# Kernel tuning notes

Measured on AMD Instinct MI355X. Metric: run time of the kernel, lower is better.

The kernel has to match this reference:

```python
import jax, jax.numpy as jnp
import numpy as np

# ---- config (matches init_kwargs) ----
B, CIN, IMG = 4, 3, 129
PATCH, STRIDE, PAD = 4, 1, 1
DIM = CIN * PATCH * PATCH          # 48, Token_performer input dim
EMB = 256                          # out_channel -> in_dim -> emb
M = EMB // 2                       # kernel_ratio=0.5 random features
UP = 2                             # up_scale
EPS = 1e-8


def layernorm(x, g, b):
    mu = x.mean(-1, keepdims=True)
    var = ((x - mu) ** 2).mean(-1, keepdims=True)
    return (x - mu) / jnp.sqrt(var + 1e-5) * g + b


def unfold(x, k=PATCH, pad=PAD):
    # torch nn.Unfold, stride=1: output [B, C*k*k, L*L], channel order (c, kh, kw)
    Bs, C, H, W = x.shape
    xp = jnp.pad(x, ((0, 0), (0, 0), (pad, pad), (pad, pad)))
    L = H + 2 * pad - k + 1
    cols = jnp.stack([xp[:, :, i:i + L, j:j + L]
                      for i in range(k) for j in range(k)], axis=2)  # [B,C,k*k,L,L]
    return cols.reshape(Bs, C * k * k, L * L)


def prm_exp(x, w):
    # Performer positive random features: exp(w@x - |x|^2/2)/sqrt(m)
    xd = 0.5 * jnp.sum(x * x, axis=-1, keepdims=True)          # [B,T,1]
    wtx = jnp.einsum('btd,md->btm', x, w)                       # [B,T,M]
    return jnp.exp(wtx - xd) / jnp.sqrt(jnp.float32(w.shape[0]))


def upsample_bilinear_ac(x, scale):
    # nn.UpsamplingBilinear2d => align_corners=True
    Bs, C, H, W = x.shape
    Ho, Wo = H * scale, W * scale
    def coords(n_in, n_out):
        f = jnp.arange(n_out, dtype=jnp.float32) * (n_in - 1) / (n_out - 1)
        i0 = jnp.clip(jnp.floor(f).astype(jnp.int32), 0, n_in - 2)
        return i0, f - i0.astype(jnp.float32)
    h0, th = coords(H, Ho)
    w0, tw = coords(W, Wo)
    xh = x[:, :, h0, :] * (1 - th)[None, None, :, None] + x[:, :, h0 + 1, :] * th[None, None, :, None]
    return xh[:, :, :, w0] * (1 - tw) + xh[:, :, :, w0 + 1] * tw


def setup_inputs() -> dict:
    key = jax.random.key(0)
    ks = jax.random.split(key, 8)
    def n(k, shape, s=0.02):
        return jax.random.normal(k, shape, dtype=jnp.float32) * s
    return dict(
        x=jax.random.normal(ks[0], (B, CIN, IMG, IMG), dtype=jnp.float32),
        g1=jnp.ones((DIM,), jnp.float32), b1=jnp.zeros((DIM,), jnp.float32),
        w_kqv=n(ks[1], (DIM, 3 * EMB)), b_kqv=jnp.zeros((3 * EMB,), jnp.float32),
        w_prm=jax.random.normal(ks[2], (M, EMB), dtype=jnp.float32) * 0.7,  # ~ orthogonal*sqrt(m)
        w_proj=n(ks[3], (EMB, EMB)), b_proj=jnp.zeros((EMB,), jnp.float32),
        g2=jnp.ones((EMB,), jnp.float32), b2=jnp.zeros((EMB,), jnp.float32),
        w_mlp1=n(ks[4], (EMB, EMB)), b_mlp1=jnp.zeros((EMB,), jnp.float32),
        w_mlp2=n(ks[5], (EMB, EMB)), b_mlp2=jnp.zeros((EMB,), jnp.float32),
    )


def reference(x, g1, b1, w_kqv, b_kqv, w_prm, w_proj, b_proj, g2, b2,
              w_mlp1, b_mlp1, w_mlp2, b_mlp2):
    Bs = x.shape[0]
    t = unfold(x).transpose(0, 2, 1)                     # [B, T, DIM], T = 128*128
    h = layernorm(t, g1, b1)
    kqv = h @ w_kqv + b_kqv                              # [B, T, 3*EMB]
    k, q, v = jnp.split(kqv, 3, axis=-1)                 # torch split order: k, q, v
    kp, qp = prm_exp(k, w_prm), prm_exp(q, w_prm)        # [B, T, M]
    D = jnp.einsum('btm,bm->bt', qp, kp.sum(axis=1))[..., None]   # [B,T,1]
    kptv = jnp.einsum('btn,btm->bnm', v, kp)             # [B, EMB, M]
    y = jnp.einsum('btm,bnm->btn', qp, kptv) / (D + EPS) # [B, T, EMB]
    y = v + (y @ w_proj + b_proj)                        # skip uses v
    z = layernorm(y, g2, b2)
    y = y + (jax.nn.gelu(z @ w_mlp1 + b_mlp1, approximate=False) @ w_mlp2 + b_mlp2)
    T = y.shape[1]
    S = int(np.sqrt(T))
    img = y.transpose(0, 2, 1).reshape(Bs, EMB, S, S)    # [B, 256, 128, 128]
    return upsample_bilinear_ac(img, UP)                 # [B, 256, 256, 256]
```

## Files before the change

kernel.cpp:

```cpp
#include <hip/hip_runtime.h>
#include <math.h>

#define TOK   16384
#define DIM   48
#define EMB   256
#define MF    128
#define IMGsz 129

typedef __attribute__((ext_vector_type(8))) short    bf16x8;
typedef __attribute__((ext_vector_type(8))) unsigned short u16x8;
typedef __attribute__((ext_vector_type(4))) unsigned short u16x4;
typedef __attribute__((ext_vector_type(4))) float    f32x4;

__device__ __forceinline__ ushort f2bf(float f) {
    union { float f; unsigned u; } v; v.f = f;
    unsigned u = v.u;
    return (ushort)((u + 0x7fffu + ((u >> 16) & 1u)) >> 16);
}
__device__ __forceinline__ float bf2f(ushort h) {
    union { unsigned u; float f; } v; v.u = ((unsigned)h) << 16; return v.f;
}

#define SWZ64(r,c)  ((r)*64  + (((((c)>>3) ^ ((r)&7)) & 7) << 3) + ((c)&7))
#define SWZ256(r,c) ((r)*256 + (((((c)>>3) ^ ((r)&7))) << 3) + ((c)&7))

__device__ __forceinline__ int fragmajor(int n, int k, int KC) {
    return (((n >> 4)*KC + (k >> 5))*4 + ((k >> 3) & 3))*128 + (n & 15)*8 + (k & 7);
}

__global__ __launch_bounds__(256) void kprep(
    const float* __restrict__ w_kqv, const float* __restrict__ b_kqv,
    const float* __restrict__ w_prm,
    const float* __restrict__ w_mlp1, const float* __restrict__ w_mlp2,
    ushort* __restrict__ Wbig, ushort* __restrict__ wT2, float* __restrict__ bkq)
{
    __shared__ float redp[64][4];
    int blk = blockIdx.x, tid = threadIdx.x;
    if (blk < 256) {
        if (tid < 64) {
            float v = (tid < DIM) ? w_kqv[tid*768 + 512 + blk] : 0.f;
            Wbig[fragmajor(blk, tid, 2)] = f2bf(v);
        }
    } else if (blk < 512) {
        int isQ = (blk >= 384);
        int m = blk - (isQ ? 384 : 256);
        int d = tid & 63, part = tid >> 6;
        float s = 0.f;
        if (d < 48) {
            const float* wr = w_kqv + d*768 + (isQ ? 256 : 0);
            const float* pr = w_prm + m*256;
            for (int n = part*64; n < part*64 + 64; n++) s += wr[n]*pr[n];
        }
        redp[d][part] = s;
        __syncthreads();
        if (tid < 64)
            Wbig[fragmajor((isQ ? 384 : 256) + m, tid, 2)] =
                f2bf(redp[tid][0]+redp[tid][1]+redp[tid][2]+redp[tid][3]);
    } else if (blk < 640) {
        int isQ = (blk >= 576);
        int j = blk - (isQ ? 576 : 512);
        int i = tid & 63, part = tid >> 6;
        int off = isQ ? 256 : 0;
        float s = 0.f;
        for (int n = part*64; n < part*64 + 64; n++) {
            float wi = (i < 48) ? w_kqv[i*768 + off + n] : (i == 48 ? b_kqv[off + n] : 0.f);
            float wj = (j < 48) ? w_kqv[j*768 + off + n] : (j == 48 ? b_kqv[off + n] : 0.f);
            s += wi*wj;
        }
        redp[i][part] = s;
        __syncthreads();
        if (tid < 64)
            Wbig[fragmajor((isQ ? 576 : 512) + j, tid, 2)] =
                f2bf(redp[tid][0]+redp[tid][1]+redp[tid][2]+redp[tid][3]);
    } else if (blk < 1152) {
        int w = (blk >= 896);
        int n = blk - (w ? 896 : 640);
        const float* src = w ? w_mlp2 : w_mlp1;
        wT2[w*65536 + fragmajor(n, tid, 8)] = f2bf(src[tid*256 + n]);
    } else {
        float s = 0.f;
        int m = tid & 127, off = (tid >= 128) ? 256 : 0;
        for (int n = 0; n < 256; n++) s += w_prm[m*256 + n]*b_kqv[off + n];
        bkq[tid] = s;
    }
}

__global__ __launch_bounds__(256, 3) void k1_mfma(
    const float* __restrict__ x, const float* __restrict__ g1, const float* __restrict__ b1,
    const ushort* __restrict__ Wbig, const float* __restrict__ b_kqv,
    const float* __restrict__ bkq,
    ushort* __restrict__ vfrag_out, ushort* __restrict__ kpT_out, ushort* __restrict__ qp_out)
{
    __shared__ __align__(16) ushort h_bf[32*64];
    __shared__ __align__(16) ushort vt_bf[32*256];
    __shared__ float xdp[4][32][2];
    __shared__ float xd2[32][2];
    __shared__ float red1[32][8], red2[32][8];
    __shared__ float mu_s[32], iv_s[32];
    float* t_s = (float*)vt_bf;

    const int blk = blockIdx.x;
    const int b  = blk >> 9;
    const int t0 = (blk & 511) << 5;
    const int tid = threadIdx.x;
    const int wid = tid >> 6;
    const int l15 = tid & 15, l4 = (tid >> 4) & 3;

    for (int e = tid; e < 32*DIM; e += 256) {
        int tok = e / DIM, j = e - tok*DIM;
        int t = t0 + tok;
        int lh = t >> 7, lw = t & 127;
        int c = j >> 4, kh = (j >> 2) & 3, kw = j & 3;
        int ih = lh + kh - 1, iw = lw + kw - 1;
        float val = 0.f;
        if (ih >= 0 && ih < IMGsz && iw >= 0 && iw < IMGsz)
            val = x[((b*3 + c)*IMGsz + ih)*IMGsz + iw];
        t_s[tok*DIM + j] = val;
    }
    __syncthreads();

    {
        int tg = tid >> 3, sl = tid & 7;
        const float* tr = &t_s[tg*DIM + sl*6];
        float s1 = 0.f, s2 = 0.f;
        #pragma unroll
        for (int j = 0; j < 6; j++) { float a = tr[j]; s1 += a; s2 = fmaf(a, a, s2); }
        red1[tg][sl] = s1; red2[tg][sl] = s2;
        __syncthreads();
        if (tid < 32) {
            float a = 0.f, q = 0.f;
            #pragma unroll
            for (int j = 0; j < 8; j++) { a += red1[tid][j]; q += red2[tid][j]; }
            float mu = a * (1.f/DIM);
            mu_s[tid] = mu;
            iv_s[tid] = rsqrtf(q*(1.f/DIM) - mu*mu + 1e-5f);
        }
        __syncthreads();
        float mu = mu_s[tg], iv = iv_s[tg];
        float hv[6];
        #pragma unroll
        for (int j = 0; j < 6; j++) hv[j] = (tr[j]-mu)*iv;
        #pragma unroll
        for (int j = 0; j < 6; j++) {
            int c = sl*6 + j;
            h_bf[SWZ64(tg, c)] = f2bf(hv[j]*g1[c] + b1[c]);
        }
        int c0 = 48 + sl*2;
        h_bf[SWZ64(tg, c0    )] = (sl == 0) ? (ushort)0x3F80 : (ushort)0;
        h_bf[SWZ64(tg, c0 + 1)] = 0;
    }
    __syncthreads();

    f32x4 acc[10][2];
    #pragma unroll
    for (int j = 0; j < 10; j++)
        #pragma unroll
        for (int m = 0; m < 2; m++) { acc[j][m][0]=0.f; acc[j][m][1]=0.f; acc[j][m][2]=0.f; acc[j][m][3]=0.f; }
    #pragma unroll
    for (int kc = 0; kc < 2; kc++) {
        int ch = ((kc*4 + l4) ^ (l15 & 7)) << 3;
        bf16x8 a0 = *(const bf16x8*)&h_bf[ l15      *64 + ch];
        bf16x8 a1 = *(const bf16x8*)&h_bf[(16 + l15)*64 + ch];
        #pragma unroll
        for (int j = 0; j < 10; j++) {
            int tile = wid + 4*j;
            bf16x8 bb = *(const bf16x8*)&Wbig[(((tile*2 + kc)*4 + l4)*16 + l15)*8];
            acc[j][0] = __builtin_amdgcn_mfma_f32_16x16x32_bf16(a0, bb, acc[j][0], 0, 0, 0);
            acc[j][1] = __builtin_amdgcn_mfma_f32_16x16x32_bf16(a1, bb, acc[j][1], 0, 0, 0);
        }
    }

    #pragma unroll
    for (int j = 0; j < 4; j++) {
        int col = (wid + 4*j)*16 + l15;
        float bias = b_kqv[512 + col];
        #pragma unroll
        for (int m = 0; m < 2; m++)
            #pragma unroll
            for (int r = 0; r < 4; r++) {
                int row = m*16 + l4*4 + r;
                vt_bf[row*256 + col] = f2bf(acc[j][m][r] + bias);
            }
    }
    #pragma unroll
    for (int m = 0; m < 2; m++)
        #pragma unroll
        for (int r = 0; r < 4; r++) {
            int row = m*16 + l4*4 + r;
            float hv = bf2f(h_bf[SWZ64(row, wid*16 + l15)]);
            float sk = acc[8][m][r]*hv, sq = acc[9][m][r]*hv;
            #pragma unroll
            for (int msk = 8; msk >= 1; msk >>= 1) {
                sk += __shfl_xor(sk, msk);
                sq += __shfl_xor(sq, msk);
            }
            if (l15 == 0) { xdp[wid][row][0] = sk; xdp[wid][row][1] = sq; }
        }
    __syncthreads();
    if (tid < 64) {
        int row = tid >> 1, ty = tid & 1;
        xd2[row][ty] = 0.5f*(xdp[0][row][ty] + xdp[1][row][ty] + xdp[2][row][ty] + xdp[3][row][ty]);
    }

    {
        ushort* dst = vfrag_out + (size_t)blk*8192 + tid*32;
        #pragma unroll
        for (int t8 = 0; t8 < 4; t8++) {
            u16x8 pk8;
            #pragma unroll
            for (int j = 0; j < 8; j++) pk8[j] = vt_bf[(t8*8 + j)*256 + tid];
            *(u16x8*)&dst[t8*8] = pk8;
        }
    }
    __syncthreads();

    const float scale = 0.08838834764831845f;
    #pragma unroll
    for (int j = 4; j < 6; j++) {
        int mcol = (wid + 4*j)*16 + l15 - 256;
        float bias = bkq[mcol];
        #pragma unroll
        for (int m = 0; m < 2; m++)
            #pragma unroll
            for (int r = 0; r < 4; r++) {
                int row = m*16 + l4*4 + r;
                vt_bf[row*256 + mcol] = f2bf(expf(acc[j][m][r] + bias - xd2[row][0]) * scale);
            }
    }
    #pragma unroll
    for (int j = 6; j < 8; j++) {
        int mcol = (wid + 4*j)*16 + l15 - 384;
        float bias = bkq[128 + mcol];
        #pragma unroll
        for (int m = 0; m < 2; m++)
            #pragma unroll
            for (int r = 0; r < 4; r++) {
                int row = m*16 + l4*4 + r;
                qp_out[(size_t)(b*TOK + t0 + row)*MF + mcol] =
                    f2bf(expf(acc[j][m][r] + bias - xd2[row][1]) * scale);
            }
    }
    __syncthreads();

    if (tid < 128) {
        ushort* dst = kpT_out + ((size_t)(b*MF + tid))*TOK + t0;
        #pragma unroll
        for (int t8 = 0; t8 < 4; t8++) {
            u16x8 pk8;
            #pragma unroll
            for (int j = 0; j < 8; j++) pk8[j] = vt_bf[(t8*8 + j)*256 + tid];
            *(u16x8*)&dst[t8*8] = pk8;
        }
    }
}

__global__ __launch_bounds__(256) void k2_ksum(const ushort* __restrict__ kpT, float* __restrict__ ksum)
{
    __shared__ float red[4];
    int blk = blockIdx.x;
    int b = blk >> 7, m = blk & 127;
    int tid = threadIdx.x;
    const ushort* row = kpT + (size_t)(b*MF + m)*TOK;
    float s = 0.f;
    for (int i = tid; i < TOK/8; i += 256) {
        u16x8 v = *(const u16x8*)&row[i*8];
        #pragma unroll
        for (int j = 0; j < 8; j++) s += bf2f(v[j]);
    }
    #pragma unroll
    for (int msk = 32; msk >= 1; msk >>= 1) s += __shfl_xor(s, msk);
    if ((tid & 63) == 0) red[tid >> 6] = s;
    __syncthreads();
    if (tid == 0) ksum[b*MF + m] = red[0] + red[1] + red[2] + red[3];
}

__global__ __launch_bounds__(256) void k3_kptv_mfma(
    const ushort* __restrict__ vfrag, const ushort* __restrict__ kpT, float* __restrict__ part)
{
    int blk = blockIdx.x;
    int b = blk >> 6, ns = (blk >> 5) & 1, kc = blk & 31;
    const int tid = threadIdx.x;
    const int wid = tid >> 6;
    const int l15 = tid & 15, l4 = (tid >> 4) & 3;
    const int t0 = kc * 512;
    const int n0 = ns*128 + wid*32;

    f32x4 acc[2][8];
    #pragma unroll
    for (int m = 0; m < 2; m++)
        #pragma unroll
        for (int n = 0; n < 8; n++) { acc[m][n][0]=0.f; acc[m][n][1]=0.f; acc[m][n][2]=0.f; acc[m][n][3]=0.f; }

    #pragma unroll
    for (int ks = 0; ks < 16; ks++) {
        int k0 = t0 + ks*32 + l4*8;
        const ushort* vt = vfrag + (size_t)(b*512 + kc*16 + ks)*8192 + l4*8;
        bf16x8 a0 = *(const bf16x8*)&vt[(n0      + l15)*32];
        bf16x8 a1 = *(const bf16x8*)&vt[(n0 + 16 + l15)*32];
        #pragma unroll
        for (int nt = 0; nt < 8; nt++) {
            bf16x8 bb = *(const bf16x8*)&kpT[((size_t)(b*MF + nt*16 + l15))*TOK + k0];
            acc[0][nt] = __builtin_amdgcn_mfma_f32_16x16x32_bf16(a0, bb, acc[0][nt], 0, 0, 0);
            acc[1][nt] = __builtin_amdgcn_mfma_f32_16x16x32_bf16(a1, bb, acc[1][nt], 0, 0, 0);
        }
    }
    #pragma unroll
    for (int mt = 0; mt < 2; mt++)
        #pragma unroll
        for (int nt = 0; nt < 8; nt++) {
            int n = n0 + mt*16 + l4*4;
            int m = nt*16 + l15;
            #pragma unroll
            for (int r = 0; r < 4; r++)
                part[(size_t)kc*131072 + (size_t)((b*EMB + n + r)*MF + m)] = acc[mt][nt][r];
        }
}

__global__ __launch_bounds__(256) void k3r_reduce(const float* __restrict__ part, float* __restrict__ kptv)
{
    int e = blockIdx.x*256 + threadIdx.x;
    float s = 0.f;
    #pragma unroll 8
    for (int kc = 0; kc < 32; kc++) s += part[(size_t)kc*131072 + e];
    kptv[e] = s;
}

__global__ __launch_bounds__(256) void k3c_combine(
    const float* __restrict__ kptv, const float* __restrict__ w_proj, ushort* __restrict__ C_bf)
{
    __shared__ float kp_s[256][8];
    int blk = blockIdx.x;
    int b = blk >> 4, m0 = (blk & 15)*8;
    int tid = threadIdx.x;

    #pragma unroll
    for (int pass = 0; pass < 8; pass++) {
        int n1 = pass*32 + (tid >> 3);
        kp_s[n1][tid & 7] = kptv[b*32768 + n1*128 + m0 + (tid & 7)];
    }
    __syncthreads();

    float acc[8];
    #pragma unroll
    for (int j = 0; j < 8; j++) acc[j] = 0.f;
    for (int n1 = 0; n1 < 256; n1++) {
        float w = w_proj[n1*256 + tid];
        #pragma unroll
        for (int j = 0; j < 8; j++) acc[j] = fmaf(kp_s[n1][j], w, acc[j]);
    }
    u16x8 pk;
    #pragma unroll
    for (int j = 0; j < 8; j++) pk[j] = f2bf(acc[j]);
    int base = (((tid >> 4)*4 + (m0 >> 5))*4 + ((m0 >> 3) & 3))*128 + (tid & 15)*8;
    *(u16x8*)&C_bf[b*32768 + base] = pk;
}

template<int K>
__device__ __forceinline__ void gemm32(const ushort* A_s, const ushort* __restrict__ B,
                                       f32x4 acc[2][4], int l15, int l4, int wid)
{
    __builtin_amdgcn_s_setprio(1);
    #pragma unroll
    for (int kc = 0; kc < (K >> 5); kc++) {
        const int ch = ((kc*4 + l4) ^ (l15 & 7)) << 3;
        bf16x8 a0 = *(const bf16x8*)&A_s[ l15      *256 + ch];
        bf16x8 a1 = *(const bf16x8*)&A_s[(16 + l15)*256 + ch];
        #pragma unroll
        for (int nt = 0; nt < 4; nt++) {
            int ntile = wid*4 + nt;
            bf16x8 bb = *(const bf16x8*)&B[(((ntile*(K >> 5) + kc)*4 + l4)*16 + l15)*8];
            acc[0][nt] = __builtin_amdgcn_mfma_f32_16x16x32_bf16(a0, bb, acc[0][nt], 0, 0, 0);
            acc[1][nt] = __builtin_amdgcn_mfma_f32_16x16x32_bf16(a1, bb, acc[1][nt], 0, 0, 0);
        }
    }
    __builtin_amdgcn_s_setprio(0);
}

__global__ __launch_bounds__(256, 4) void k4_attn_tail(
    const ushort* __restrict__ qp, const ushort* __restrict__ vfrag,
    const float* __restrict__ ksum, const ushort* __restrict__ C_bf,
    const ushort* __restrict__ wT2,
    const float* __restrict__ b_proj,
    const float* __restrict__ g2, const float* __restrict__ b2,
    const float* __restrict__ b_mlp1, const float* __restrict__ b_mlp2,
    ushort* __restrict__ img2b)
{
    __shared__ __align__(16) ushort A_s[16448];
    __shared__ float D_s[32];
    __shared__ float redD[32][8];
    __shared__ float red1[4][32], red2[4][32];
    __shared__ float mu_s[32], iv_s[32];

    const int blk = blockIdx.x;
    const int b  = blk >> 9;
    const int t0 = (blk & 511) << 5;
    const int tid = threadIdx.x;
    const int wid = tid >> 6;
    const int lane = tid & 63;
    const int l15 = lane & 15, l4 = lane >> 4;

    u16x4 vreg[8];
    {
        const ushort* vf = vfrag + (size_t)blk*8192 + l4*4;
        #pragma unroll
        for (int nt = 0; nt < 4; nt++)
            #pragma unroll
            for (int m = 0; m < 2; m++)
                vreg[nt*2 + m] = *(const u16x4*)&vf[(wid*64 + nt*16 + l15)*32 + m*16];
    }
    float bp[4];
    #pragma unroll
    for (int nt = 0; nt < 4; nt++) bp[nt] = b_proj[wid*64 + nt*16 + l15];

    {
        int tk = tid >> 3, seg = tid & 7;
        const ushort* qrow = qp + (size_t)(b*TOK + t0 + tk)*MF + seg*16;
        u16x8 q0 = *(const u16x8*)&qrow[0];
        u16x8 q1 = *(const u16x8*)&qrow[8];
        const float* ks = ksum + b*MF + seg*16;
        float dd = 0.f;
        #pragma unroll
        for (int j = 0; j < 8; j++) {
            dd = fmaf(bf2f(q0[j]), ks[j],   dd);
            dd = fmaf(bf2f(q1[j]), ks[j+8], dd);
        }
        redD[tk][seg] = dd;
        int xr = tk & 7;
        *(u16x8*)&A_s[tk*256 + (((seg*2  ) ^ xr) << 3)] = q0;
        *(u16x8*)&A_s[tk*256 + (((seg*2+1) ^ xr) << 3)] = q1;
    }
    __syncthreads();
    if (tid < 32) {
        float s = 0.f;
        #pragma unroll
        for (int j = 0; j < 8; j++) s += redD[tid][j];
        D_s[tid] = s + 1e-8f;
    }

    f32x4 acc[2][4];
    #define ZACC() { _Pragma("unroll") for (int m_=0;m_<2;m_++) _Pragma("unroll") for (int n_=0;n_<4;n_++) { acc[m_][n_][0]=0.f;acc[m_][n_][1]=0.f;acc[m_][n_][2]=0.f;acc[m_][n_][3]=0.f; } }

    ZACC();
    gemm32<MF>(A_s, C_bf + (size_t)b*32768, acc, l15, l4, wid);
    __syncthreads();
    float y2[2][4][4];
    #pragma unroll
    for (int nt = 0; nt < 4; nt++) {
        #pragma unroll
        for (int m = 0; m < 2; m++)
            #pragma unroll
            for (int r = 0; r < 4; r++) {
                int row = m*16 + l4*4 + r;
                y2[m][nt][r] = acc[m][nt][r]/D_s[row] + bp[nt] + bf2f(vreg[nt*2 + m][r]);
            }
    }

    {
        #pragma unroll
        for (int m = 0; m < 2; m++)
            #pragma unroll
            for (int r = 0; r < 4; r++) {
                float s1 = 0.f, s2 = 0.f;
                #pragma unroll
                for (int nt = 0; nt < 4; nt++) {
                    float a = y2[m][nt][r];
                    s1 += a; s2 = fmaf(a, a, s2);
                }
                #pragma unroll
                for (int msk = 8; msk >= 1; msk >>= 1) {
                    s1 += __shfl_xor(s1, msk);
                    s2 += __shfl_xor(s2, msk);
                }
                if (l15 == 0) {
                    int row = m*16 + l4*4 + r;
                    red1[wid][row] = s1; red2[wid][row] = s2;
                }
            }
        __syncthreads();
        if (tid < 32) {
            float a = red1[0][tid] + red1[1][tid] + red1[2][tid] + red1[3][tid];
            float q = red2[0][tid] + red2[1][tid] + red2[2][tid] + red2[3][tid];
            float mu = a * (1.f/EMB);
            mu_s[tid] = mu;
            iv_s[tid] = rsqrtf(q*(1.f/EMB) - mu*mu + 1e-5f);
        }
        __syncthreads();
        #pragma unroll
        for (int nt = 0; nt < 4; nt++) {
            int col = wid*64 + nt*16 + l15;
            float gg = g2[col], bb = b2[col];
            #pragma unroll
            for (int m = 0; m < 2; m++)
                #pragma unroll
                for (int r = 0; r < 4; r++) {
                    int row = m*16 + l4*4 + r;
                    A_s[SWZ256(row, col)] = f2bf((y2[m][nt][r] - mu_s[row])*iv_s[row]*gg + bb);
                }
        }
    }
    __syncthreads();

    ZACC();
    gemm32<EMB>(A_s, wT2, acc, l15, l4, wid);
    __syncthreads();
    #pragma unroll
    for (int nt = 0; nt < 4; nt++) {
        int col = wid*64 + nt*16 + l15;
        float bm = b_mlp1[col];
        #pragma unroll
        for (int m = 0; m < 2; m++)
            #pragma unroll
            for (int r = 0; r < 4; r++) {
                int row = m*16 + l4*4 + r;
                float a = acc[m][nt][r] + bm;
                A_s[SWZ256(row, col)] = f2bf(0.5f*a*(1.f + erff(a*0.70710678118654752f)));
            }
    }
    __syncthreads();

    ZACC();
    gemm32<EMB>(A_s, wT2 + 65536, acc, l15, l4, wid);
    #pragma unroll
    for (int nt = 0; nt < 4; nt++) {
        int col = wid*64 + nt*16 + l15;
        float bm = b_mlp2[col];
        #pragma unroll
        for (int m = 0; m < 2; m++)
            #pragma unroll
            for (int r = 0; r < 4; r++)
                y2[m][nt][r] += acc[m][nt][r] + bm;
    }
    __syncthreads();

    float* A_f = (float*)A_s;
    #pragma unroll
    for (int nt = 0; nt < 4; nt++) {
        int col = wid*64 + nt*16 + l15;
        #pragma unroll
        for (int m = 0; m < 2; m++)
            #pragma unroll
            for (int r = 0; r < 4; r++)
                A_f[(m*16 + l4*4 + r)*257 + col] = y2[m][nt][r];
    }
    __syncthreads();
    {
        int tq = tid & 7, cb = tid >> 3;
        #pragma unroll
        for (int pass = 0; pass < 8; pass++) {
            int c = pass*32 + cb;
            u16x4 pk;
            #pragma unroll
            for (int j = 0; j < 4; j++) pk[j] = f2bf(A_f[(tq*4 + j)*257 + c]);
            *(u16x4*)&img2b[((size_t)(b*EMB + c))*TOK + t0 + tq*4] = pk;
        }
    }
}

__global__ __launch_bounds__(256) void k6_upsample(const ushort* __restrict__ img2b, float* __restrict__ out)
{
    int idx = blockIdx.x*256 + threadIdx.x;
    int wq = idx & 63;
    int ho = (idx >> 6) & 255;
    int c  = (idx >> 14) & 255;
    int b  = idx >> 22;
    const float sc = 127.f/255.f;
    float fh = ho * sc; int h0 = (int)fh; if (h0 > 126) h0 = 126; float th = fh - h0;
    int wo = wq*4;
    int w0[4]; float tw[4];
    #pragma unroll
    for (int j = 0; j < 4; j++) {
        float fw = (wo + j) * sc;
        int w = (int)fw; if (w > 126) w = 126;
        w0[j] = w; tw[j] = fw - w;
    }
    int wsrt = w0[0] > 124 ? 124 : w0[0];
    const ushort* p = img2b + (((size_t)(b*EMB + c))*128 + h0)*128 + wsrt;
    float r0[4], r1[4];
    #pragma unroll
    for (int j = 0; j < 4; j++) { r0[j] = bf2f(p[j]); r1[j] = bf2f(p[128 + j]); }
    f32x4 o;
    #pragma unroll
    for (int j = 0; j < 4; j++) {
        int i = w0[j] - wsrt;
        float a00 = (i == 0) ? r0[0] : ((i == 1) ? r0[1] : r0[2]);
        float a01 = (i == 0) ? r0[1] : ((i == 1) ? r0[2] : r0[3]);
        float a10 = (i == 0) ? r1[0] : ((i == 1) ? r1[1] : r1[2]);
        float a11 = (i == 0) ? r1[1] : ((i == 1) ? r1[2] : r1[3]);
        float top = fmaf(a01 - a00, tw[j], a00);
        float bot = fmaf(a11 - a10, tw[j], a10);
        o[j] = fmaf(bot - top, th, top);
    }
    *(f32x4*)&out[(size_t)idx*4] = o;
}

extern "C" void kernel_launch(void* const* d_in, const int* in_sizes, int n_in,
                              void* d_out, int out_size, void* d_ws, size_t ws_size,
                              hipStream_t stream)
{
    const float* x      = (const float*)d_in[0];
    const float* g1     = (const float*)d_in[1];
    const float* b1     = (const float*)d_in[2];
    const float* w_kqv  = (const float*)d_in[3];
    const float* b_kqv  = (const float*)d_in[4];
    const float* w_prm  = (const float*)d_in[5];
    const float* w_proj = (const float*)d_in[6];
    const float* b_proj = (const float*)d_in[7];
    const float* g2     = (const float*)d_in[8];
    const float* b2     = (const float*)d_in[9];
    const float* w_mlp1 = (const float*)d_in[10];
    const float* b_mlp1 = (const float*)d_in[11];
    const float* w_mlp2 = (const float*)d_in[12];
    const float* b_mlp2 = (const float*)d_in[13];
    float* out = (float*)d_out;
    float* ws  = (float*)d_ws;

    ushort* vfrag    = (ushort*)(ws);
    ushort* qp_bf    = (ushort*)(ws + 8388608);
    ushort* kpT_bf   = (ushort*)(ws + 12582912);
    ushort* img2b    = (ushort*)(ws + 16777216);
    float*  ksum     = ws + 25165824;
    ushort* Wbig     = (ushort*)(ws + 25166336);
    ushort* wT2      = (ushort*)(ws + 25186816);
    float*  bkq      = ws + 25252352;
    float*  kptv_f32 = ws + 25252608;
    ushort* C_bf     = (ushort*)(ws + 25383680);
    float*  part     = ws + 25416448;

    hipLaunchKernelGGL(kprep, dim3(1153), dim3(256), 0, stream,
                       w_kqv, b_kqv, w_prm, w_mlp1, w_mlp2, Wbig, wT2, bkq);
    hipLaunchKernelGGL(k1_mfma, dim3(2048), dim3(256), 0, stream,
                       x, g1, b1, Wbig, b_kqv, bkq, vfrag, kpT_bf, qp_bf);
    hipLaunchKernelGGL(k2_ksum, dim3(512), dim3(256), 0, stream, kpT_bf, ksum);
    hipLaunchKernelGGL(k3_kptv_mfma, dim3(256), dim3(256), 0, stream, vfrag, kpT_bf, part);
    hipLaunchKernelGGL(k3r_reduce, dim3(512), dim3(256), 0, stream, part, kptv_f32);
    hipLaunchKernelGGL(k3c_combine, dim3(64), dim3(256), 0, stream, kptv_f32, w_proj, C_bf);
    hipLaunchKernelGGL(k4_attn_tail, dim3(2048), dim3(256), 0, stream,
                       qp_bf, vfrag, ksum, C_bf, wT2, b_proj, g2, b2,
                       b_mlp1, b_mlp2, img2b);
    hipLaunchKernelGGL(k6_upsample, dim3(65536), dim3(256), 0, stream, img2b, out);
}
```

Baseline: 261.9 us.

## Fuse ksum into kptv kernel, stage kp/qp in LDS, batch upsample work

Removes the separate k2_ksum kernel and computes per-chunk key-feature sums inside the kptv MFMA kernel, then reduces them in k3r_reduce. In k1, the kp and qp exp features go to dedicated LDS buffers so qp can be written out with coalesced 16-byte stores instead of scattered 2-byte stores, and one barrier is dropped. The upsample kernel now handles 8 output quads per thread with one-eighth as many blocks. The extra LDS in k1 may reduce occupancy at the requested 3 blocks per CU.

```diff
diff --git a/kernel.cpp b/kernel.cpp
--- a/kernel.cpp
+++ b/kernel.cpp
@@ -93,8 +93,9 @@
 {
     __shared__ __align__(16) ushort h_bf[32*64];
     __shared__ __align__(16) ushort vt_bf[32*256];
+    __shared__ __align__(16) ushort kp_s[32*128];
+    __shared__ __align__(16) ushort qp_s[32*128];
     __shared__ float xdp[4][32][2];
-    __shared__ float xd2[32][2];
     __shared__ float red1[32][8], red2[32][8];
     __shared__ float mu_s[32], iv_s[32];
     float* t_s = (float*)vt_bf;
@@ -197,10 +198,26 @@
             if (l15 == 0) { xdp[wid][row][0] = sk; xdp[wid][row][1] = sq; }
         }
     __syncthreads();
-    if (tid < 64) {
-        int row = tid >> 1, ty = tid & 1;
-        xd2[row][ty] = 0.5f*(xdp[0][row][ty] + xdp[1][row][ty] + xdp[2][row][ty] + xdp[3][row][ty]);
-    }
+
+    const float scale = 0.08838834764831845f;
+    #pragma unroll
+    for (int m = 0; m < 2; m++)
+        #pragma unroll
+        for (int r = 0; r < 4; r++) {
+            int row = m*16 + l4*4 + r;
+            float xdk = 0.5f*(xdp[0][row][0]+xdp[1][row][0]+xdp[2][row][0]+xdp[3][row][0]);
+            float xdq = 0.5f*(xdp[0][row][1]+xdp[1][row][1]+xdp[2][row][1]+xdp[3][row][1]);
+            #pragma unroll
+            for (int j = 4; j < 6; j++) {
+                int mcol = wid*16 + (j-4)*64 + l15;
+                kp_s[row*128 + mcol] = f2bf(expf(acc[j][m][r] + bkq[mcol] - xdk) * scale);
+            }
+            #pragma unroll
+            for (int j = 6; j < 8; j++) {
+                int mcol = wid*16 + (j-6)*64 + l15;
+                qp_s[row*128 + mcol] = f2bf(expf(acc[j][m][r] + bkq[128 + mcol] - xdq) * scale);
+            }
+        }
 
     {
         ushort* dst = vfrag_out + (size_t)blk*8192 + tid*32;
@@ -214,68 +231,29 @@
     }
     __syncthreads();
 
-    const float scale = 0.08838834764831845f;
-    #pragma unroll
-    for (int j = 4; j < 6; j++) {
-        int mcol = (wid + 4*j)*16 + l15 - 256;
-        float bias = bkq[mcol];
-        #pragma unroll
-        for (int m = 0; m < 2; m++)
-            #pragma unroll
-            for (int r = 0; r < 4; r++) {
-                int row = m*16 + l4*4 + r;
-                vt_bf[row*256 + mcol] = f2bf(expf(acc[j][m][r] + bias - xd2[row][0]) * scale);
-            }
-    }
-    #pragma unroll
-    for (int j = 6; j < 8; j++) {
-        int mcol = (wid + 4*j)*16 + l15 - 384;
-        float bias = bkq[128 + mcol];
-        #pragma unroll
-        for (int m = 0; m < 2; m++)
-            #pragma unroll
-            for (int r = 0; r < 4; r++) {
-                int row = m*16 + l4*4 + r;
-                qp_out[(size_t)(b*TOK + t0 + row)*MF + mcol] =
-                    f2bf(expf(acc[j][m][r] + bias - xd2[row][1]) * scale);
-            }
-    }
-    __syncthreads();
-
     if (tid < 128) {
         ushort* dst = kpT_out + ((size_t)(b*MF + tid))*TOK + t0;
         #pragma unroll
         for (int t8 = 0; t8 < 4; t8++) {
             u16x8 pk8;
             #pragma unroll
-            for (int j = 0; j < 8; j++) pk8[j] = vt_bf[(t8*8 + j)*256 + tid];
+            for (int j = 0; j < 8; j++) pk8[j] = kp_s[(t8*8 + j)*128 + tid];
             *(u16x8*)&dst[t8*8] = pk8;
         }
     }
-}
-
-__global__ __launch_bounds__(256) void k2_ksum(const ushort* __restrict__ kpT, float* __restrict__ ksum)
-{
-    __shared__ float red[4];
-    int blk = blockIdx.x;
-    int b = blk >> 7, m = blk & 127;
-    int tid = threadIdx.x;
-    const ushort* row = kpT + (size_t)(b*MF + m)*TOK;
-    float s = 0.f;
-    for (int i = tid; i < TOK/8; i += 256) {
-        u16x8 v = *(const u16x8*)&row[i*8];
-        #pragma unroll
-        for (int j = 0; j < 8; j++) s += bf2f(v[j]);
-    }
-    #pragma unroll
-    for (int msk = 32; msk >= 1; msk >>= 1) s += __shfl_xor(s, msk);
-    if ((tid & 63) == 0) red[tid >> 6] = s;
-    __syncthreads();
-    if (tid == 0) ksum[b*MF + m] = red[0] + red[1] + red[2] + red[3];
+    {
+        int tk = tid >> 3, seg = tid & 7;
+        ushort* dst = qp_out + (size_t)(b*TOK + t0 + tk)*MF + seg*16;
+        u16x8 a = *(const u16x8*)&qp_s[tk*128 + seg*16];
+        u16x8 c = *(const u16x8*)&qp_s[tk*128 + seg*16 + 8];
+        *(u16x8*)&dst[0] = a;
+        *(u16x8*)&dst[8] = c;
+    }
 }
 
 __global__ __launch_bounds__(256) void k3_kptv_mfma(
-    const ushort* __restrict__ vfrag, const ushort* __restrict__ kpT, float* __restrict__ part)
+    const ushort* __restrict__ vfrag, const ushort* __restrict__ kpT,
+    float* __restrict__ part, float* __restrict__ ksump)
 {
     int blk = blockIdx.x;
     int b = blk >> 6, ns = (blk >> 5) & 1, kc = blk & 31;
@@ -284,12 +262,16 @@
     const int l15 = tid & 15, l4 = (tid >> 4) & 3;
     const int t0 = kc * 512;
     const int n0 = ns*128 + wid*32;
+    const bool doks = (ns == 0) && (wid == 0);
 
     f32x4 acc[2][8];
     #pragma unroll
     for (int m = 0; m < 2; m++)
         #pragma unroll
         for (int n = 0; n < 8; n++) { acc[m][n][0]=0.f; acc[m][n][1]=0.f; acc[m][n][2]=0.f; acc[m][n][3]=0.f; }
+    float sks[8];
+    #pragma unroll
+    for (int n = 0; n < 8; n++) sks[n] = 0.f;
 
     #pragma unroll
     for (int ks = 0; ks < 16; ks++) {
@@ -300,8 +282,22 @@
         #pragma unroll
         for (int nt = 0; nt < 8; nt++) {
             bf16x8 bb = *(const bf16x8*)&kpT[((size_t)(b*MF + nt*16 + l15))*TOK + k0];
+            if (doks) {
+                #pragma unroll
+                for (int j = 0; j < 8; j++) sks[nt] += bf2f((ushort)bb[j]);
+            }
             acc[0][nt] = __builtin_amdgcn_mfma_f32_16x16x32_bf16(a0, bb, acc[0][nt], 0, 0, 0);
             acc[1][nt] = __builtin_amdgcn_mfma_f32_16x16x32_bf16(a1, bb, acc[1][nt], 0, 0, 0);
+        }
+    }
+    if (doks) {
+        #pragma unroll
+        for (int nt = 0; nt < 8; nt++) {
+            float s = sks[nt];
+            s += __shfl_xor(s, 16);
+            s += __shfl_xor(s, 32);
+            if (l4 == 0 && tid < 64)
+                ksump[(size_t)(b*32 + kc)*128 + nt*16 + l15] = s;
         }
     }
     #pragma unroll
@@ -316,13 +312,24 @@
         }
 }
 
-__global__ __launch_bounds__(256) void k3r_reduce(const float* __restrict__ part, float* __restrict__ kptv)
-{
-    int e = blockIdx.x*256 + threadIdx.x;
+__global__ __launch_bounds__(256) void k3r_reduce(
+    const float* __restrict__ part, const float* __restrict__ ksump,
+    float* __restrict__ kptv, float* __restrict__ ksum)
+{
+    int blk = blockIdx.x;
+    int e = blk*256 + threadIdx.x;
     float s = 0.f;
     #pragma unroll 8
     for (int kc = 0; kc < 32; kc++) s += part[(size_t)kc*131072 + e];
     kptv[e] = s;
+    if (blk < 2) {
+        int i = blk*256 + threadIdx.x;
+        int b = i >> 7, m = i & 127;
+        float t = 0.f;
+        #pragma unroll 8
+        for (int kc = 0; kc < 32; kc++) t += ksump[(size_t)(b*32 + kc)*128 + m];
+        ksum[i] = t;
+    }
 }
 
 __global__ __launch_bounds__(256) void k3c_combine(
@@ -558,39 +565,42 @@
 
 __global__ __launch_bounds__(256) void k6_upsample(const ushort* __restrict__ img2b, float* __restrict__ out)
 {
-    int idx = blockIdx.x*256 + threadIdx.x;
-    int wq = idx & 63;
-    int ho = (idx >> 6) & 255;
-    int c  = (idx >> 14) & 255;
-    int b  = idx >> 22;
-    const float sc = 127.f/255.f;
-    float fh = ho * sc; int h0 = (int)fh; if (h0 > 126) h0 = 126; float th = fh - h0;
-    int wo = wq*4;
-    int w0[4]; float tw[4];
-    #pragma unroll
-    for (int j = 0; j < 4; j++) {
-        float fw = (wo + j) * sc;
-        int w = (int)fw; if (w > 126) w = 126;
-        w0[j] = w; tw[j] = fw - w;
-    }
-    int wsrt = w0[0] > 124 ? 124 : w0[0];
-    const ushort* p = img2b + (((size_t)(b*EMB + c))*128 + h0)*128 + wsrt;
-    float r0[4], r1[4];
-    #pragma unroll
-    for (int j = 0; j < 4; j++) { r0[j] = bf2f(p[j]); r1[j] = bf2f(p[128 + j]); }
-    f32x4 o;
-    #pragma unroll
-    for (int j = 0; j < 4; j++) {
-        int i = w0[j] - wsrt;
-        float a00 = (i == 0) ? r0[0] : ((i == 1) ? r0[1] : r0[2]);
-        float a01 = (i == 0) ? r0[1] : ((i == 1) ? r0[2] : r0[3]);
-        float a10 = (i == 0) ? r1[0] : ((i == 1) ? r1[1] : r1[2]);
-        float a11 = (i == 0) ? r1[1] : ((i == 1) ? r1[2] : r1[3]);
-        float top = fmaf(a01 - a00, tw[j], a00);
-        float bot = fmaf(a11 - a10, tw[j], a10);
-        o[j] = fmaf(bot - top, th, top);
-    }
-    *(f32x4*)&out[(size_t)idx*4] = o;
+    #pragma unroll
+    for (int it = 0; it < 8; it++) {
+        int idx = blockIdx.x*2048 + it*256 + threadIdx.x;
+        int wq = idx & 63;
+        int ho = (idx >> 6) & 255;
+        int c  = (idx >> 14) & 255;
+        int b  = idx >> 22;
+        const float sc = 127.f/255.f;
+        float fh = ho * sc; int h0 = (int)fh; if (h0 > 126) h0 = 126; float th = fh - h0;
+        int wo = wq*4;
+        int w0[4]; float tw[4];
+        #pragma unroll
+        for (int j = 0; j < 4; j++) {
+            float fw = (wo + j) * sc;
+            int w = (int)fw; if (w > 126) w = 126;
+            w0[j] = w; tw[j] = fw - w;
+        }
+        int wsrt = w0[0] > 124 ? 124 : w0[0];
+        const ushort* p = img2b + (((size_t)(b*EMB + c))*128 + h0)*128 + wsrt;
+        float r0[4], r1[4];
+        #pragma unroll
+        for (int j = 0; j < 4; j++) { r0[j] = bf2f(p[j]); r1[j] = bf2f(p[128 + j]); }
+        f32x4 o;
+        #pragma unroll
+        for (int j = 0; j < 4; j++) {
+            int i = w0[j] - wsrt;
+            float a00 = (i == 0) ? r0[0] : ((i == 1) ? r0[1] : r0[2]);
+            float a01 = (i == 0) ? r0[1] : ((i == 1) ? r0[2] : r0[3]);
+            float a10 = (i == 0) ? r1[0] : ((i == 1) ? r1[1] : r1[2]);
+            float a11 = (i == 0) ? r1[1] : ((i == 1) ? r1[2] : r1[3]);
+            float top = fmaf(a01 - a00, tw[j], a00);
+            float bot = fmaf(a11 - a10, tw[j], a10);
+            o[j] = fmaf(bot - top, th, top);
+        }
+        *(f32x4*)&out[(size_t)idx*4] = o;
+    }
 }
 
 extern "C" void kernel_launch(void* const* d_in, const int* in_sizes, int n_in,
@@ -624,18 +634,18 @@
     float*  bkq      = ws + 25252352;
     float*  kptv_f32 = ws + 25252608;
     ushort* C_bf     = (ushort*)(ws + 25383680);
-    float*  part     = ws + 25416448;
+    float*  ksump    = ws + 25416448;
+    float*  part     = ws + 25432832;
 
     hipLaunchKernelGGL(kprep, dim3(1153), dim3(256), 0, stream,
                        w_kqv, b_kqv, w_prm, w_mlp1, w_mlp2, Wbig, wT2, bkq);
     hipLaunchKernelGGL(k1_mfma, dim3(2048), dim3(256), 0, stream,
                        x, g1, b1, Wbig, b_kqv, bkq, vfrag, kpT_bf, qp_bf);
-    hipLaunchKernelGGL(k2_ksum, dim3(512), dim3(256), 0, stream, kpT_bf, ksum);
-    hipLaunchKernelGGL(k3_kptv_mfma, dim3(256), dim3(256), 0, stream, vfrag, kpT_bf, part);
-    hipLaunchKernelGGL(k3r_reduce, dim3(512), dim3(256), 0, stream, part, kptv_f32);
+    hipLaunchKernelGGL(k3_kptv_mfma, dim3(256), dim3(256), 0, stream, vfrag, kpT_bf, part, ksump);
+    hipLaunchKernelGGL(k3r_reduce, dim3(512), dim3(256), 0, stream, part, ksump, kptv_f32, ksum);
     hipLaunchKernelGGL(k3c_combine, dim3(64), dim3(256), 0, stream, kptv_f32, w_proj, C_bf);
     hipLaunchKernelGGL(k4_attn_tail, dim3(2048), dim3(256), 0, stream,
                        qp_bf, vfrag, ksum, C_bf, wT2, b_proj, g2, b2,
                        b_mlp1, b_mlp2, img2b);
-    hipLaunchKernelGGL(k6_upsample, dim3(65536), dim3(256), 0, stream, img2b, out);
-}
+    hipLaunchKernelGGL(k6_upsample, dim3(8192), dim3(256), 0, stream, img2b, out);
+}
```

Measured after the change: 266.5 us. No clear change (+1.8%).
